# Kernel tuning notes

Measured on AMD Instinct MI355X. Metric: run time of the kernel, lower is better.

## Reference

```python
import jax, jax.numpy as jnp
import numpy as np

T = 100      # sequence length / output times
B = 2048     # batch
DT = 0.02    # euler step == spacing of ts -> one step per interval
CLAMP = 6.0
LOG2PI = float(np.log(2.0 * np.pi))
sp = jax.nn.softplus


def setup_inputs() -> dict:
    key = jax.random.key(0)
    ks = jax.random.split(key, 20)
    rn = lambda k, s, sc=1.0: jax.random.normal(k, s, dtype=jnp.float32) * sc
    inp = {}
    inp['xs'] = rn(ks[0], (T, B, 3, 50))
    inp['ts'] = jnp.arange(T, dtype=jnp.float32) * DT
    inp['eps0'] = rn(ks[1], (B, 6))
    inp['dW'] = rn(ks[2], (T - 1, B, 6)) * np.sqrt(DT)  # Brownian increments ~ N(0, dt)
    # encoder: 150->30->30->15
    inp['eW1'] = rn(ks[3], (150, 30), 150 ** -0.5); inp['eb1'] = jnp.zeros((30,), jnp.float32)
    inp['eW2'] = rn(ks[4], (30, 30), 30 ** -0.5);   inp['eb2'] = jnp.zeros((30,), jnp.float32)
    inp['eW3'] = rn(ks[5], (30, 15), 30 ** -0.5);   inp['eb3'] = jnp.zeros((15,), jnp.float32)
    # decoder: 6->30->30->100
    inp['dcW1'] = rn(ks[6], (6, 30), 6 ** -0.5);    inp['dcb1'] = jnp.zeros((30,), jnp.float32)
    inp['dcW2'] = rn(ks[7], (30, 30), 30 ** -0.5);  inp['dcb2'] = jnp.zeros((30,), jnp.float32)
    inp['dcW3'] = rn(ks[8], (30, 100), 30 ** -0.5); inp['dcb3'] = jnp.zeros((100,), jnp.float32)
    # f_net: (6+1+3)=10 -> 30 -> 6
    inp['fW1'] = rn(ks[9], (10, 30), 10 ** -0.5);   inp['fb1'] = jnp.zeros((30,), jnp.float32)
    inp['fW2'] = rn(ks[10], (30, 6), 30 ** -0.5);   inp['fb2'] = jnp.zeros((6,), jnp.float32)
    # h_net: (6+1)=7 -> 30 -> 6
    inp['hW1'] = rn(ks[11], (7, 30), 7 ** -0.5);    inp['hb1'] = jnp.zeros((30,), jnp.float32)
    inp['hW2'] = rn(ks[12], (30, 6), 30 ** -0.5);   inp['hb2'] = jnp.zeros((6,), jnp.float32)
    # 6 g_nets stacked: 2 -> 30 -> 1 (sigmoid)
    inp['gW1'] = rn(ks[13], (6, 2, 30), 2 ** -0.5); inp['gb1'] = jnp.zeros((6, 30), jnp.float32)
    inp['gW2'] = rn(ks[14], (6, 30, 1), 30 ** -0.5); inp['gb2'] = jnp.zeros((6, 1), jnp.float32)
    inp['pz0_mean'] = jnp.zeros((1, 6), jnp.float32)
    inp['pz0_logstd'] = jnp.zeros((1, 6), jnp.float32)
    return inp


def _forward(xs, ts, eps0, dW, eW1, eb1, eW2, eb2, eW3, eb3,
             dcW1, dcb1, dcW2, dcb2, dcW3, dcb3,
             fW1, fb1, fW2, fb2, hW1, hb1, hW2, hb2,
             gW1, gb1, gW2, gb2, pz0_mean, pz0_logstd):
    # ---- encoder on time-reversed xs ----
    xse = jnp.flip(xs, 0).reshape(T, B, 150)
    e = sp(xse @ eW1 + eb1)
    e = sp(e @ eW2 + eb2)
    e = e @ eW3 + eb3                         # [T,B,15]
    qz0_mean = e[-1, :, :6]
    qz0_logstd = e[-1, :, 6:12]
    ctx = jnp.flip(e[..., 12:15], 0)           # [T,B,3]

    z0 = qz0_mean + jnp.exp(jnp.clip(qz0_logstd, -CLAMP, CLAMP)) * eps0

    # ---- Euler-Maruyama with logqp (one step per ts interval) ----
    def step(z, sc):
        k, dWk = sc
        t = ts[k]
        dtk = ts[k + 1] - ts[k]
        c = ctx[jnp.minimum(k + 1, T - 1)]     # searchsorted(ts, t, right=True) clamped
        tb = jnp.broadcast_to(t, (B, 1)).astype(z.dtype)
        f = sp(jnp.concatenate([tb, z, c], 1) @ fW1 + fb1) @ fW2 + fb2
        h = sp(jnp.concatenate([tb, z], 1) @ hW1 + hb1) @ hW2 + hb2
        gin = jnp.stack([jnp.broadcast_to(t, (B, 6)).astype(z.dtype), z], -1)  # [B,6,2]
        gh = sp(jnp.einsum('bdi,dih->bdh', gin, gW1) + gb1)
        g = jax.nn.sigmoid(jnp.einsum('bdh,dho->bdo', gh, gW2) + gb2)[..., 0]  # [B,6]
        u = (f - h) / g
        logr = 0.5 * jnp.sum(u * u, axis=1) * dtk   # [B]
        zn = z + f * dtk + g * dWk
        return zn, (zn, logr)

    _, (zs_tail, log_ratio) = jax.lax.scan(step, z0, (jnp.arange(T - 1), dW))
    zs = jnp.concatenate([z0[None], zs_tail], 0)   # [T,B,6]

    # ---- decoder + likelihood ----
    d = sp(zs @ dcW1 + dcb1)
    d = sp(d @ dcW2 + dcb2)
    d = d @ dcW3 + dcb3                        # [T,B,100]
    xm, xl = d[..., :50], d[..., 50:]
    xsig = jnp.exp(jnp.clip(xl, -CLAMP, CLAMP))
    tgt = xs[:, :, -1, :]
    lp = -0.5 * ((tgt - xm) / xsig) ** 2 - jnp.log(xsig) - 0.5 * LOG2PI
    log_pxs = jnp.mean(jnp.sum(lp, axis=(0, 2)))

    # ---- KL(q(z0)||p(z0)) + path term ----
    sq = jnp.exp(jnp.clip(qz0_logstd, -CLAMP, CLAMP))
    spz = jnp.exp(jnp.clip(pz0_logstd, -CLAMP, CLAMP))
    kl = jnp.log(spz / sq) + (sq ** 2 + (qz0_mean - pz0_mean) ** 2) / (2.0 * spz ** 2) - 0.5
    logqp0 = jnp.mean(jnp.sum(kl, axis=1))
    logqp_path = jnp.mean(jnp.sum(log_ratio, axis=0))
    return log_pxs, logqp0 + logqp_path


def reference(xs, ts, eps0, dW, eW1, eb1, eW2, eb2, eW3, eb3,
              dcW1, dcb1, dcW2, dcb2, dcW3, dcb3,
              fW1, fb1, fW2, fb2, hW1, hb1, hW2, hb2,
              gW1, gb1, gW2, gb2, pz0_mean, pz0_logstd):
    return _forward(xs, ts, eps0, dW, eW1, eb1, eW2, eb2, eW3, eb3,
                    dcW1, dcb1, dcW2, dcb2, dcW3, dcb3,
                    fW1, fb1, fW2, fb2, hW1, hb1, hW2, hb2,
                    gW1, gb1, gW2, gb2, pz0_mean, pz0_logstd)
```

## Files before the change

### kernel.cpp

```cpp
#include <hip/hip_runtime.h>
#include <hip/hip_bf16.h>
#include <math.h>

#define Tn 100
#define Bn 2048

typedef int v2i __attribute__((ext_vector_type(2)));
typedef _Float16 h2v __attribute__((ext_vector_type(2)));

__device__ __forceinline__ float sp_f(float x) {
    float e = __expf(-fabsf(x));
    return fmaxf(x, 0.f) + __logf(1.f + e);
}
__device__ __forceinline__ float clamp6(float x) {
    return fminf(fmaxf(x, -6.f), 6.f);
}
__device__ __forceinline__ unsigned int packh2(float a, float b) {
    h2v h; h.x = (_Float16)a; h.y = (_Float16)b;
    return __builtin_bit_cast(unsigned int, h);
}
__device__ __forceinline__ float dot2f(unsigned int a, unsigned int b, float c) {
#if __has_builtin(__builtin_amdgcn_fdot2)
    return __builtin_amdgcn_fdot2(__builtin_bit_cast(h2v, a),
                                  __builtin_bit_cast(h2v, b), c, false);
#else
    h2v ha = __builtin_bit_cast(h2v, a), hb = __builtin_bit_cast(h2v, b);
    return fmaf((float)ha.y, (float)hb.y, fmaf((float)ha.x, (float)hb.x, c));
#endif
}

__device__ __forceinline__ float dpp_xor1(float x) {
    return __int_as_float(__builtin_amdgcn_mov_dpp(__float_as_int(x), 0xB1, 0xF, 0xF, 1));
}
__device__ __forceinline__ float dpp_xor2(float x) {
    return __int_as_float(__builtin_amdgcn_mov_dpp(__float_as_int(x), 0x4E, 0xF, 0xF, 1));
}
__device__ __forceinline__ float dpp_hmirror(float x) {
    return __int_as_float(__builtin_amdgcn_mov_dpp(__float_as_int(x), 0x141, 0xF, 0xF, 1));
}
__device__ __forceinline__ float dpp_ror8(float x) {
    return __int_as_float(__builtin_amdgcn_mov_dpp(__float_as_int(x), 0x128, 0xF, 0xF, 1));
}
template <int OFF>
__device__ __forceinline__ float swz(float x) {
    return __int_as_float(__builtin_amdgcn_ds_swizzle(__float_as_int(x), OFF));
}
__device__ __forceinline__ float xor16_sum(float x) {
#if __has_builtin(__builtin_amdgcn_permlane16_swap)
    v2i r = __builtin_amdgcn_permlane16_swap(__float_as_int(x), __float_as_int(x), false, false);
    return __int_as_float(r[0]) + __int_as_float(r[1]);
#else
    return x + swz<0x401F>(x);
#endif
}
__device__ __forceinline__ float other_half(float x) {
#if __has_builtin(__builtin_amdgcn_permlane32_swap)
    v2i r = __builtin_amdgcn_permlane32_swap(__float_as_int(x), __float_as_int(x), false, false);
    return (__int_as_float(r[0]) + __int_as_float(r[1])) - x;
#else
    return __shfl_xor(x, 32);
#endif
}

__device__ __forceinline__ void rowd2(float* ha, float* hb, const unsigned int* wrow,
                                      unsigned int xa, unsigned int xb) {
#pragma unroll
    for (int q = 0; q < 7; ++q) {
        uint4 wv = *(const uint4*)(wrow + 4 * q);
        ha[4 * q + 0] = dot2f(xa, wv.x, ha[4 * q + 0]);
        hb[4 * q + 0] = dot2f(xb, wv.x, hb[4 * q + 0]);
        ha[4 * q + 1] = dot2f(xa, wv.y, ha[4 * q + 1]);
        hb[4 * q + 1] = dot2f(xb, wv.y, hb[4 * q + 1]);
        ha[4 * q + 2] = dot2f(xa, wv.z, ha[4 * q + 2]);
        hb[4 * q + 2] = dot2f(xb, wv.z, hb[4 * q + 2]);
        ha[4 * q + 3] = dot2f(xa, wv.w, ha[4 * q + 3]);
        hb[4 * q + 3] = dot2f(xb, wv.w, hb[4 * q + 3]);
    }
    uint2 wt = *(const uint2*)(wrow + 28);
    ha[28] = dot2f(xa, wt.x, ha[28]);
    hb[28] = dot2f(xb, wt.x, hb[28]);
    ha[29] = dot2f(xa, wt.y, ha[29]);
    hb[29] = dot2f(xb, wt.y, hb[29]);
}
__device__ __forceinline__ void dot30_2(const float* ha, const float* hb,
                                        const float* wrow, float& ra, float& rb) {
    float a0 = 0.f, a1 = 0.f, b0 = 0.f, b1 = 0.f;
#pragma unroll
    for (int q = 0; q < 7; ++q) {
        float4 wv = *(const float4*)(wrow + 4 * q);
        a0 = fmaf(ha[4 * q + 0], wv.x, a0);
        b0 = fmaf(hb[4 * q + 0], wv.x, b0);
        a1 = fmaf(ha[4 * q + 1], wv.y, a1);
        b1 = fmaf(hb[4 * q + 1], wv.y, b1);
        a0 = fmaf(ha[4 * q + 2], wv.z, a0);
        b0 = fmaf(hb[4 * q + 2], wv.z, b0);
        a1 = fmaf(ha[4 * q + 3], wv.w, a1);
        b1 = fmaf(hb[4 * q + 3], wv.w, b1);
    }
    float2 wt = *(const float2*)(wrow + 28);
    a0 = fmaf(ha[28], wt.x, a0);
    b0 = fmaf(hb[28], wt.x, b0);
    a1 = fmaf(ha[29], wt.y, a1);
    b1 = fmaf(hb[29], wt.y, b1);
    ra = a0 + a1; rb = b0 + b1;
}
__device__ __forceinline__ void dot16p_2(const unsigned int* pa, const unsigned int* pb,
                                         const unsigned int* wrow, float& ra, float& rb) {
    float a0 = 0.f, a1 = 0.f, b0 = 0.f, b1 = 0.f;
#pragma unroll
    for (int q = 0; q < 4; ++q) {
        uint4 wv = *(const uint4*)(wrow + 4 * q);
        a0 = dot2f(pa[4 * q + 0], wv.x, a0);
        b0 = dot2f(pb[4 * q + 0], wv.x, b0);
        a1 = dot2f(pa[4 * q + 1], wv.y, a1);
        b1 = dot2f(pb[4 * q + 1], wv.y, b1);
        a0 = dot2f(pa[4 * q + 2], wv.z, a0);
        b0 = dot2f(pb[4 * q + 2], wv.z, b0);
        a1 = dot2f(pa[4 * q + 3], wv.w, a1);
        b1 = dot2f(pb[4 * q + 3], wv.w, b1);
    }
    ra = a0 + a1; rb = b0 + b1;
}

#define ENC_LOAD2(b0, b1, base)                                               \
    _Pragma("unroll")                                                         \
    for (int i = 0; i < 5; ++i) {                                             \
        b0[i] = *(const float2*)(x0 + (base) + 2 * i);                        \
        b1[i] = *(const float2*)(x1 + (base) + 2 * i);                        \
    }
#define ENC_COMP2(b0, b1, pb)                                                 \
    _Pragma("unroll")                                                         \
    for (int i = 0; i < 5; ++i) {                                             \
        unsigned int xa = packh2(b0[i].x, b0[i].y);                           \
        unsigned int xb = packh2(b1[i].x, b1[i].y);                           \
        rowd2(h1a, h1b, &wh1[((pb) + i) * 32], xa, xb);                       \
    }

__global__ __launch_bounds__(256) void enc_kernel(
    const float* __restrict__ xs,
    const float* __restrict__ eW1, const float* __restrict__ eb1,
    const float* __restrict__ eW2, const float* __restrict__ eb2,
    const float* __restrict__ eW3, const float* __restrict__ eb3,
    float* __restrict__ ctx, float* __restrict__ qm, float* __restrict__ qs)
{
    __shared__ __align__(16) unsigned int wh1[75 * 32];
    __shared__ __align__(16) unsigned int wh2[15 * 32];
    __shared__ __align__(16) float wf[555];

    for (int i = threadIdx.x; i < 75 * 30; i += 256) {
        int p = i / 30, j = i % 30;
        wh1[p * 32 + j] = packh2(eW1[(2 * p) * 30 + j], eW1[(2 * p + 1) * 30 + j]);
    }
    for (int i = threadIdx.x; i < 15 * 30; i += 256) {
        int p = i / 30, j = i % 30;
        wh2[p * 32 + j] = packh2(eW2[(2 * p) * 30 + j], eW2[(2 * p + 1) * 30 + j]);
    }
    if (threadIdx.x < 30) wf[threadIdx.x] = eb1[threadIdx.x];
    if (threadIdx.x >= 32 && threadIdx.x < 62) wf[30 + threadIdx.x - 32] = eb2[threadIdx.x - 32];
    for (int i = threadIdx.x; i < 90; i += 256) {
        int o = i / 30, j2 = i % 30;
        wf[60 + o * 32 + j2] = eW3[j2 * 15 + 12 + o];
    }
    for (int i = threadIdx.x; i < 360; i += 256) {
        int o = i / 30, j2 = i % 30;
        wf[156 + o * 32 + j2] = eW3[j2 * 15 + o];
    }
    if (threadIdx.x >= 64 && threadIdx.x < 79) wf[540 + threadIdx.x - 64] = eb3[threadIdx.x - 64];
    __syncthreads();

    int t = threadIdx.x;
    size_t base = (size_t)blockIdx.x * 512;
    size_t s0 = base + t, s1 = base + t + 256;
    const float* x0 = xs + s0 * 150;
    const float* x1 = xs + s1 * 150;

    float h1a[30], h1b[30];
#pragma unroll
    for (int j = 0; j < 30; ++j) { h1a[j] = wf[j]; h1b[j] = h1a[j]; }

    float2 A0[5], A1[5], B0[5], B1[5];
    ENC_LOAD2(A0, A1, 0)
    ENC_LOAD2(B0, B1, 10)
    int fb = 0;
#pragma unroll 1
    for (int it = 0; it < 6; ++it) {
        ENC_COMP2(A0, A1, fb / 2)
        ENC_LOAD2(A0, A1, fb + 20)
        ENC_COMP2(B0, B1, fb / 2 + 5)
        ENC_LOAD2(B0, B1, fb + 30)
        fb += 20;
    }
    ENC_COMP2(A0, A1, 60)
    ENC_LOAD2(A0, A1, 140)
    ENC_COMP2(B0, B1, 65)
    ENC_COMP2(A0, A1, 70)

#pragma unroll
    for (int j = 0; j < 30; ++j) { h1a[j] = sp_f(h1a[j]); h1b[j] = sp_f(h1b[j]); }

    unsigned int p1a[15], p1b[15];
#pragma unroll
    for (int p = 0; p < 15; ++p) {
        p1a[p] = packh2(h1a[2 * p], h1a[2 * p + 1]);
        p1b[p] = packh2(h1b[2 * p], h1b[2 * p + 1]);
    }
    float h2a[30], h2b[30];
#pragma unroll
    for (int j = 0; j < 30; ++j) { h2a[j] = wf[30 + j]; h2b[j] = h2a[j]; }
#pragma unroll
    for (int p = 0; p < 15; ++p)
        rowd2(h2a, h2b, &wh2[p * 32], p1a[p], p1b[p]);
#pragma unroll
    for (int j = 0; j < 30; ++j) { h2a[j] = sp_f(h2a[j]); h2b[j] = sp_f(h2b[j]); }

    float oa3[3], ob3[3];
#pragma unroll
    for (int o = 0; o < 3; ++o) {
        float ra, rb;
        dot30_2(h2a, h2b, &wf[60 + o * 32], ra, rb);
        oa3[o] = wf[540 + 12 + o] + ra;
        ob3[o] = wf[540 + 12 + o] + rb;
    }
    float* cp0 = ctx + s0 * 3;
    cp0[0] = oa3[0]; cp0[1] = oa3[1]; cp0[2] = oa3[2];
    float* cp1 = ctx + s1 * 3;
    cp1[0] = ob3[0]; cp1[1] = ob3[1]; cp1[2] = ob3[2];

    if (blockIdx.x < 4) {
#pragma unroll
        for (int o = 0; o < 12; ++o) {
            float ra, rb;
            dot30_2(h2a, h2b, &wf[156 + o * 32], ra, rb);
            float va = wf[540 + o] + ra, vb = wf[540 + o] + rb;
            if (o < 6) { qm[s0 * 6 + o] = va; qm[s1 * 6 + o] = vb; }
            else       { qs[s0 * 6 + o - 6] = va; qs[s1 * 6 + o - 6] = vb; }
        }
    }
}

__global__ __launch_bounds__(128, 4) void scan_kernel(
    const float* __restrict__ ts, const float* __restrict__ dWall,
    const float* __restrict__ fW1, const float* __restrict__ fb1,
    const float* __restrict__ fW2, const float* __restrict__ fb2,
    const float* __restrict__ hW1, const float* __restrict__ hb1,
    const float* __restrict__ hW2, const float* __restrict__ hb2,
    const float* __restrict__ gW1, const float* __restrict__ gb1,
    const float* __restrict__ gW2, const float* __restrict__ gb2,
    const float* __restrict__ ctx,
    const float* __restrict__ qm, const float* __restrict__ qs,
    const float* __restrict__ eps0, const float* __restrict__ pm,
    const float* __restrict__ ps,
    float* __restrict__ zsb, float* __restrict__ acc)
{
    int tid = threadIdx.x;
    int lane = tid & 63;
    int b = blockIdx.x;
    bool isA = tid < 64;

    __shared__ float sRec[99 * 12];
    __shared__ float exF[2][12];
    __shared__ float exG[2][8];

    for (int i = tid; i < 99 * 3; i += 128) {
        int k = i / 3, e = i % 3;
        float2 v = *(const float2*)(dWall + ((size_t)k * Bn + b) * 6 + e * 2);
        *(float2*)&sRec[k * 12 + e * 2] = v;
    }
    for (int i = tid; i < 99 * 3; i += 128) {
        int k = i / 3, e = i % 3;
        sRec[k * 12 + 6 + e] = ctx[((size_t)(k + 1) * Bn + b) * 3 + e];
    }
    for (int i = tid; i < 99; i += 128) {
        float t0 = ts[i], t1 = ts[i + 1];
        sRec[i * 12 + 9]  = 0.f;
        sRec[i * 12 + 10] = t0;
        sRec[i * 12 + 11] = t1 - t0;
    }

    float z[6];
    float zq = 0.f;
    float wl1[10], b1w, wl2[6], fb2v[6], hb2v[6];
    float gwa[4], gwb[4], gw2v[4], gbb[4], gb2v = 0.f, wselq = 0.f;
    int dL = 0;

    if (isA) {
        bool lower = lane < 32;
        int j = lane & 31;
        int jc = (j < 30) ? j : 29;
        bool jvalid = (j < 30);
#pragma unroll
        for (int i = 0; i < 10; ++i)
            wl1[i] = lower ? fW1[i * 30 + jc] : (i < 7 ? hW1[i * 30 + jc] : 0.f);
        b1w = lower ? fb1[jc] : hb1[jc];
#pragma unroll
        for (int d = 0; d < 6; ++d)
            wl2[d] = jvalid ? (lower ? fW2[jc * 6 + d] : hW2[jc * 6 + d]) : 0.f;
#pragma unroll
        for (int d = 0; d < 6; ++d) { fb2v[d] = fb2[d]; hb2v[d] = hb2[d]; }
#pragma unroll
        for (int d = 0; d < 6; ++d) {
            float m = qm[b * 6 + d];
            float sq = __expf(clamp6(qs[b * 6 + d]));
            z[d] = fmaf(sq, eps0[b * 6 + d], m);
        }
        if (tid == 0) {
            float* zp = zsb + (size_t)b * 6;
            *(float2*)(zp)     = make_float2(z[0], z[1]);
            *(float2*)(zp + 2) = make_float2(z[2], z[3]);
            *(float2*)(zp + 4) = make_float2(z[4], z[5]);
        }
    } else {
        int dL8 = lane >> 3;
        dL = (dL8 < 6) ? dL8 : 0;
        wselq = (dL8 < 6) ? 0.0625f : 0.f;
        int s = lane & 7;
#pragma unroll
        for (int u = 0; u < 4; ++u) {
            int jj = s + 8 * u;
            bool ok = (dL8 < 6) && (jj < 30);
            gwa[u]  = ok ? gW1[dL * 60 + jj] : 0.f;
            gwb[u]  = ok ? gW1[dL * 60 + 30 + jj] : 0.f;
            gw2v[u] = ok ? gW2[dL * 30 + jj] : 0.f;
            gbb[u]  = ok ? gb1[dL * 30 + jj] : 0.f;
        }
        gb2v = gb2[dL];
        {
            float m = qm[b * 6 + dL];
            float sq = __expf(clamp6(qs[b * 6 + dL]));
            zq = fmaf(sq, eps0[b * 6 + dL], m);
        }
        if (tid == 64) {
            float klsum = 0.f;
#pragma unroll
            for (int d = 0; d < 6; ++d) {
                float m = qm[b * 6 + d];
                float sq = __expf(clamp6(qs[b * 6 + d]));
                float spz = __expf(clamp6(ps[d]));
                float dm = m - pm[d];
                klsum += __logf(spz / sq) + (sq * sq + dm * dm) / (2.f * spz * spz) - 0.5f;
            }
            atomicAdd(&acc[1], klsum);
        }
    }

    __syncthreads();

    float pacc = 0.f;

    for (int k = 0; k < Tn - 1; ++k) {
        int kb = k & 1;

        if (isA) {
            float4 r0 = *(float4*)&sRec[k * 12];
            float4 r1 = *(float4*)&sRec[k * 12 + 4];
            float4 r2 = *(float4*)&sRec[k * 12 + 8];
            float t = r2.z, dt = r2.w;

            float a = fmaf(t, wl1[0], b1w);
#pragma unroll
            for (int i = 0; i < 6; ++i) a = fmaf(z[i], wl1[1 + i], a);
            a = fmaf(r1.z, wl1[7], a);
            a = fmaf(r1.w, wl1[8], a);
            a = fmaf(r2.x, wl1[9], a);
            float hid = sp_f(a);

            float pp[6];
#pragma unroll
            for (int d = 0; d < 6; ++d) pp[d] = hid * wl2[d];
#pragma unroll
            for (int d = 0; d < 6; ++d) pp[d] += dpp_xor1(pp[d]);
#pragma unroll
            for (int d = 0; d < 6; ++d) pp[d] += dpp_xor2(pp[d]);
#pragma unroll
            for (int d = 0; d < 6; ++d) pp[d] += dpp_hmirror(pp[d]);
#pragma unroll
            for (int d = 0; d < 6; ++d) pp[d] += dpp_ror8(pp[d]);
#pragma unroll
            for (int d = 0; d < 6; ++d) pp[d] = xor16_sum(pp[d]);
            float fvv[6], dfh[6];
            bool lower = lane < 32;
#pragma unroll
            for (int d = 0; d < 6; ++d) {
                float oth = other_half(pp[d]);
                float fsum = lower ? pp[d] : oth;
                float hsum = lower ? oth : pp[d];
                fvv[d] = fsum + fb2v[d];
                dfh[d] = fvv[d] - (hsum + hb2v[d]);
            }
            if (lane == 0) {
                *(float4*)&exF[kb][0] = make_float4(fvv[0], fvv[1], fvv[2], fvv[3]);
                *(float4*)&exF[kb][4] = make_float4(fvv[4], fvv[5], dfh[0], dfh[1]);
                *(float4*)&exF[kb][8] = make_float4(dfh[2], dfh[3], dfh[4], dfh[5]);
            }

            __syncthreads();

            float4 g03 = *(float4*)&exG[kb][0];
            float2 g45 = *(float2*)&exG[kb][4];
            float gl[6] = { g03.x, g03.y, g03.z, g03.w, g45.x, g45.y };
            float dwv[6] = { r0.x, r0.y, r0.z, r0.w, r1.x, r1.y };
#pragma unroll
            for (int d = 0; d < 6; ++d)
                z[d] = fmaf(gl[d], dwv[d], fmaf(fvv[d], dt, z[d]));

            if (tid == 0) {
                float* zp = zsb + ((size_t)(k + 1) * Bn + b) * 6;
                *(float2*)(zp)     = make_float2(z[0], z[1]);
                *(float2*)(zp + 2) = make_float2(z[2], z[3]);
                *(float2*)(zp + 4) = make_float2(z[4], z[5]);
            }
        } else {
            float2 tdt = *(float2*)&sRec[k * 12 + 10];
            float t = tdt.x, dt = tdt.y;
            float dwq = sRec[k * 12 + dL];

            float ga = 0.f;
#pragma unroll
            for (int u = 0; u < 4; ++u) {
                float pre = fmaf(t, gwa[u], gbb[u]);
                pre = fmaf(zq, gwb[u], pre);
                ga = fmaf(sp_f(pre), gw2v[u], ga);
            }
            ga += dpp_xor1(ga);
            ga += dpp_xor2(ga);
            ga += dpp_hmirror(ga);
            float gacc = ga + gb2v;
            float e = __expf(-gacc);
            float rg = 1.f + e;
            float gval = __builtin_amdgcn_rcpf(rg);
            if ((lane & 7) == 0 && (lane >> 3) < 6)
                exG[kb][dL] = gval;

            __syncthreads();

            float fq  = exF[kb][dL];
            float dfq = exF[kb][6 + dL];
            float u = dfq * rg;
            pacc = fmaf(wselq * dt, u * u, pacc);
            zq = fmaf(gval, dwq, fmaf(fq, dt, zq));
        }
    }
    if (!isA) {
#pragma unroll
        for (int mm = 1; mm <= 32; mm <<= 1) pacc += __shfl_xor(pacc, mm);
        if (tid == 64) atomicAdd(&acc[2], pacc);
    }
}

#define DEC_TLOAD(b0, b1, base)                                               \
    _Pragma("unroll")                                                         \
    for (int i = 0; i < 5; ++i) {                                             \
        b0[i] = *(const float2*)(tg0 + (base) + 2 * i);                       \
        b1[i] = *(const float2*)(tg1 + (base) + 2 * i);                       \
    }
#define DEC_LCOMP(b0, b1, base)                                               \
    _Pragma("unroll")                                                         \
    for (int i = 0; i < 10; ++i) {                                            \
        int ff = (base) + i;                                                  \
        float dma, dmb, dla, dlb;                                             \
        dot16p_2(p2a, p2b, &wh3[ff * 16], dma, dmb);                          \
        dot16p_2(p2a, p2b, &wh3[(50 + ff) * 16], dla, dlb);                   \
        float xma = wd[256 + ff] + dma, xmb = wd[256 + ff] + dmb;             \
        float cla = clamp6(wd[256 + 50 + ff] + dla);                          \
        float clb = clamp6(wd[256 + 50 + ff] + dlb);                          \
        float tva = (i & 1) ? b0[i >> 1].y : b0[i >> 1].x;                    \
        float tvb = (i & 1) ? b1[i >> 1].y : b1[i >> 1].x;                    \
        float ua = (tva - xma) * __expf(-cla);                                \
        float ub = (tvb - xmb) * __expf(-clb);                                \
        lpa += -0.5f * ua * ua - cla - 0.91893853320467274f;                  \
        lpb += -0.5f * ub * ub - clb - 0.91893853320467274f;                  \
    }

__global__ __launch_bounds__(256) void dec_kernel(
    const float* __restrict__ zsb, const float* __restrict__ xs,
    const float* __restrict__ dcW1, const float* __restrict__ dcb1,
    const float* __restrict__ dcW2, const float* __restrict__ dcb2,
    const float* __restrict__ dcW3, const float* __restrict__ dcb3,
    float* __restrict__ acc)
{
    __shared__ __align__(16) float wd[356];
    __shared__ __align__(16) unsigned int wh2d[15 * 32];
    __shared__ __align__(16) unsigned int wh3[100 * 16];

    for (int i = threadIdx.x; i < 180; i += 256) wd[(i / 30) * 32 + (i % 30)] = dcW1[i];
    if (threadIdx.x < 30) wd[192 + threadIdx.x] = dcb1[threadIdx.x];
    if (threadIdx.x >= 32 && threadIdx.x < 62) wd[224 + threadIdx.x - 32] = dcb2[threadIdx.x - 32];
    for (int i = threadIdx.x; i < 100; i += 256) wd[256 + i] = dcb3[i];
    for (int i = threadIdx.x; i < 15 * 30; i += 256) {
        int p = i / 30, j = i % 30;
        wh2d[p * 32 + j] = packh2(dcW2[(2 * p) * 30 + j], dcW2[(2 * p + 1) * 30 + j]);
    }
    for (int i = threadIdx.x; i < 100 * 16; i += 256) {
        int ff = i / 16, p = i % 16;
        wh3[i] = (p < 15) ? packh2(dcW3[(2 * p) * 100 + ff], dcW3[(2 * p + 1) * 100 + ff]) : 0u;
    }
    __syncthreads();

    int t = threadIdx.x;
    size_t base = (size_t)blockIdx.x * 512;
    size_t s0 = base + t, s1 = base + t + 256;

    float za[6], zb[6];
    {
        const float* zp0 = zsb + s0 * 6;
        const float* zp1 = zsb + s1 * 6;
#pragma unroll
        for (int i = 0; i < 3; ++i) {
            float2 v0 = *(const float2*)(zp0 + 2 * i);
            float2 v1 = *(const float2*)(zp1 + 2 * i);
            za[2 * i] = v0.x; za[2 * i + 1] = v0.y;
            zb[2 * i] = v1.x; zb[2 * i + 1] = v1.y;
        }
    }

    float h1a[30], h1b[30];
#pragma unroll
    for (int j = 0; j < 30; ++j) { h1a[j] = wd[192 + j]; h1b[j] = h1a[j]; }
#pragma unroll
    for (int i = 0; i < 6; ++i) {
        float via = za[i], vib = zb[i];
        const float* wrow = &wd[i * 32];
#pragma unroll
        for (int q = 0; q < 7; ++q) {
            float4 wv = *(const float4*)(wrow + 4 * q);
            h1a[4 * q + 0] = fmaf(via, wv.x, h1a[4 * q + 0]);
            h1b[4 * q + 0] = fmaf(vib, wv.x, h1b[4 * q + 0]);
            h1a[4 * q + 1] = fmaf(via, wv.y, h1a[4 * q + 1]);
            h1b[4 * q + 1] = fmaf(vib, wv.y, h1b[4 * q + 1]);
            h1a[4 * q + 2] = fmaf(via, wv.z, h1a[4 * q + 2]);
            h1b[4 * q + 2] = fmaf(vib, wv.z, h1b[4 * q + 2]);
            h1a[4 * q + 3] = fmaf(via, wv.w, h1a[4 * q + 3]);
            h1b[4 * q + 3] = fmaf(vib, wv.w, h1b[4 * q + 3]);
        }
        float2 wt = *(const float2*)(wrow + 28);
        h1a[28] = fmaf(via, wt.x, h1a[28]);
        h1b[28] = fmaf(vib, wt.x, h1b[28]);
        h1a[29] = fmaf(via, wt.y, h1a[29]);
        h1b[29] = fmaf(vib, wt.y, h1b[29]);
    }
#pragma unroll
    for (int j = 0; j < 30; ++j) { h1a[j] = sp_f(h1a[j]); h1b[j] = sp_f(h1b[j]); }

    unsigned int p1a[15], p1b[15];
#pragma unroll
    for (int p = 0; p < 15; ++p) {
        p1a[p] = packh2(h1a[2 * p], h1a[2 * p + 1]);
        p1b[p] = packh2(h1b[2 * p], h1b[2 * p + 1]);
    }
    float h2a[30], h2b[30];
#pragma unroll
    for (int j = 0; j < 30; ++j) { h2a[j] = wd[224 + j]; h2b[j] = h2a[j]; }
#pragma unroll
    for (int p = 0; p < 15; ++p)
        rowd2(h2a, h2b, &wh2d[p * 32], p1a[p], p1b[p]);
#pragma unroll
    for (int j = 0; j < 30; ++j) { h2a[j] = sp_f(h2a[j]); h2b[j] = sp_f(h2b[j]); }

    unsigned int p2a[16], p2b[16];
#pragma unroll
    for (int p = 0; p < 15; ++p) {
        p2a[p] = packh2(h2a[2 * p], h2a[2 * p + 1]);
        p2b[p] = packh2(h2b[2 * p], h2b[2 * p + 1]);
    }
    p2a[15] = 0u; p2b[15] = 0u;

    const float* tg0 = xs + s0 * 150 + 100;
    const float* tg1 = xs + s1 * 150 + 100;
    float lpa = 0.f, lpb = 0.f;
    float2 TA0[5], TA1[5], TB0[5], TB1[5];
    DEC_TLOAD(TA0, TA1, 0)
    DEC_TLOAD(TB0, TB1, 10)
    DEC_LCOMP(TA0, TA1, 0)
    DEC_TLOAD(TA0, TA1, 20)
    DEC_LCOMP(TB0, TB1, 10)
    DEC_TLOAD(TB0, TB1, 30)
    DEC_LCOMP(TA0, TA1, 20)
    DEC_TLOAD(TA0, TA1, 40)
    DEC_LCOMP(TB0, TB1, 30)
    DEC_LCOMP(TA0, TA1, 40)

    float lpacc = lpa + lpb;
#pragma unroll
    for (int mm = 1; mm <= 32; mm <<= 1) lpacc += __shfl_xor(lpacc, mm);
    __shared__ float red[4];
    if ((threadIdx.x & 63) == 0) red[threadIdx.x >> 6] = lpacc;
    __syncthreads();
    if (threadIdx.x == 0) atomicAdd(&acc[0], red[0] + red[1] + red[2] + red[3]);
}

__global__ void final_kernel(const float* __restrict__ acc, float* __restrict__ out)
{
    out[0] = acc[0] * (1.f / (float)Bn);
    out[1] = (acc[1] + acc[2]) * (1.f / (float)Bn);
}

extern "C" void kernel_launch(void* const* d_in, const int* in_sizes, int n_in,
                              void* d_out, int out_size, void* d_ws, size_t ws_size,
                              hipStream_t stream)
{
    const float* xs   = (const float*)d_in[0];
    const float* ts   = (const float*)d_in[1];
    const float* eps0 = (const float*)d_in[2];
    const float* dW   = (const float*)d_in[3];
    const float* eW1  = (const float*)d_in[4];
    const float* eb1  = (const float*)d_in[5];
    const float* eW2  = (const float*)d_in[6];
    const float* eb2  = (const float*)d_in[7];
    const float* eW3  = (const float*)d_in[8];
    const float* eb3  = (const float*)d_in[9];
    const float* dcW1 = (const float*)d_in[10];
    const float* dcb1 = (const float*)d_in[11];
    const float* dcW2 = (const float*)d_in[12];
    const float* dcb2 = (const float*)d_in[13];
    const float* dcW3 = (const float*)d_in[14];
    const float* dcb3 = (const float*)d_in[15];
    const float* fW1  = (const float*)d_in[16];
    const float* fb1  = (const float*)d_in[17];
    const float* fW2  = (const float*)d_in[18];
    const float* fb2  = (const float*)d_in[19];
    const float* hW1  = (const float*)d_in[20];
    const float* hb1  = (const float*)d_in[21];
    const float* hW2  = (const float*)d_in[22];
    const float* hb2  = (const float*)d_in[23];
    const float* gW1  = (const float*)d_in[24];
    const float* gb1  = (const float*)d_in[25];
    const float* gW2  = (const float*)d_in[26];
    const float* gb2  = (const float*)d_in[27];
    const float* pm   = (const float*)d_in[28];
    const float* ps   = (const float*)d_in[29];

    float* ws  = (float*)d_ws;
    float* acc = ws;
    float* ctx = ws + 16;
    float* qm  = ctx + 614400;
    float* qs  = qm + 12288;
    float* zs  = qs + 12288;
    float* out = (float*)d_out;

    hipMemsetAsync(acc, 0, 16 * sizeof(float), stream);
    enc_kernel<<<400, 256, 0, stream>>>(xs, eW1, eb1, eW2, eb2, eW3, eb3, ctx, qm, qs);
    scan_kernel<<<2048, 128, 0, stream>>>(ts, dW, fW1, fb1, fW2, fb2, hW1, hb1,
                                          hW2, hb2, gW1, gb1, gW2, gb2, ctx,
                                          qm, qs, eps0, pm, ps, zs, acc);
    dec_kernel<<<400, 256, 0, stream>>>(zs, xs, dcW1, dcb1, dcW2, dcb2, dcW3, dcb3, acc);
    final_kernel<<<1, 1, 0, stream>>>(acc, out);
}
```

Baseline: 244.0 us.

## Process two batch elements per scan block to add ILP and halve syncs

Each scan block now advances two independent SDE trajectories at once, interleaving their f/h and g network evaluations, and the grid shrinks from 2048 to 1024 blocks. This is meant to hide the latency of the serial per-step dependency chain (DPP reductions, transcendentals, barriers) with independent work, and to halve the total number of block-level barriers. The cost is higher register and LDS use per thread, which may lower occupancy, and fewer blocks to spread across the CUs. The first-layer dot product is also split into two partial accumulators to shorten the dependency chain.

After: 253.3 us. 3.8% more time.

```diff
diff --git a/kernel.cpp b/kernel.cpp
--- a/kernel.cpp
+++ b/kernel.cpp
@@ -254,31 +254,30 @@
 {
     int tid = threadIdx.x;
     int lane = tid & 63;
-    int b = blockIdx.x;
+    int b0c = blockIdx.x * 2;
     bool isA = tid < 64;
 
-    __shared__ float sRec[99 * 12];
-    __shared__ float exF[2][12];
-    __shared__ float exG[2][8];
-
-    for (int i = tid; i < 99 * 3; i += 128) {
-        int k = i / 3, e = i % 3;
-        float2 v = *(const float2*)(dWall + ((size_t)k * Bn + b) * 6 + e * 2);
-        *(float2*)&sRec[k * 12 + e * 2] = v;
-    }
-    for (int i = tid; i < 99 * 3; i += 128) {
-        int k = i / 3, e = i % 3;
-        sRec[k * 12 + 6 + e] = ctx[((size_t)(k + 1) * Bn + b) * 3 + e];
+    __shared__ float sRec[99 * 24];
+    __shared__ float exF[2][2][12];
+    __shared__ float exG[2][2][8];
+
+    for (int i = tid; i < 99 * 6; i += 128) {
+        int k = i / 6, r = i % 6, c = r / 3, e = r % 3;
+        float2 v = *(const float2*)(dWall + ((size_t)k * Bn + b0c + c) * 6 + e * 2);
+        *(float2*)&sRec[k * 24 + c * 12 + e * 2] = v;
+    }
+    for (int i = tid; i < 99 * 6; i += 128) {
+        int k = i / 6, r = i % 6, c = r / 3, e = r % 3;
+        sRec[k * 24 + c * 12 + 6 + e] = ctx[((size_t)(k + 1) * Bn + b0c + c) * 3 + e];
     }
     for (int i = tid; i < 99; i += 128) {
         float t0 = ts[i], t1 = ts[i + 1];
-        sRec[i * 12 + 9]  = 0.f;
-        sRec[i * 12 + 10] = t0;
-        sRec[i * 12 + 11] = t1 - t0;
-    }
-
-    float z[6];
-    float zq = 0.f;
+        sRec[i * 24 + 9]  = 0.f; sRec[i * 24 + 10] = t0; sRec[i * 24 + 11] = t1 - t0;
+        sRec[i * 24 + 21] = 0.f; sRec[i * 24 + 22] = t0; sRec[i * 24 + 23] = t1 - t0;
+    }
+
+    float z0[6], z1[6];
+    float zq0 = 0.f, zq1 = 0.f;
     float wl1[10], b1w, wl2[6], fb2v[6], hb2v[6];
     float gwa[4], gwb[4], gw2v[4], gbb[4], gb2v = 0.f, wselq = 0.f;
     int dL = 0;
@@ -299,15 +298,18 @@
         for (int d = 0; d < 6; ++d) { fb2v[d] = fb2[d]; hb2v[d] = hb2[d]; }
 #pragma unroll
         for (int d = 0; d < 6; ++d) {
-            float m = qm[b * 6 + d];
-            float sq = __expf(clamp6(qs[b * 6 + d]));
-            z[d] = fmaf(sq, eps0[b * 6 + d], m);
+            float m0 = qm[b0c * 6 + d];
+            float s0 = __expf(clamp6(qs[b0c * 6 + d]));
+            z0[d] = fmaf(s0, eps0[b0c * 6 + d], m0);
+            float m1 = qm[(b0c + 1) * 6 + d];
+            float s1 = __expf(clamp6(qs[(b0c + 1) * 6 + d]));
+            z1[d] = fmaf(s1, eps0[(b0c + 1) * 6 + d], m1);
         }
         if (tid == 0) {
-            float* zp = zsb + (size_t)b * 6;
-            *(float2*)(zp)     = make_float2(z[0], z[1]);
-            *(float2*)(zp + 2) = make_float2(z[2], z[3]);
-            *(float2*)(zp + 4) = make_float2(z[4], z[5]);
+            float* zp = zsb + (size_t)b0c * 6;
+            *(float4*)(zp)     = make_float4(z0[0], z0[1], z0[2], z0[3]);
+            *(float4*)(zp + 4) = make_float4(z0[4], z0[5], z1[0], z1[1]);
+            *(float4*)(zp + 8) = make_float4(z1[2], z1[3], z1[4], z1[5]);
         }
     } else {
         int dL8 = lane >> 3;
@@ -325,19 +327,25 @@
         }
         gb2v = gb2[dL];
         {
-            float m = qm[b * 6 + dL];
-            float sq = __expf(clamp6(qs[b * 6 + dL]));
-            zq = fmaf(sq, eps0[b * 6 + dL], m);
+            float m0 = qm[b0c * 6 + dL];
+            float s0 = __expf(clamp6(qs[b0c * 6 + dL]));
+            zq0 = fmaf(s0, eps0[b0c * 6 + dL], m0);
+            float m1 = qm[(b0c + 1) * 6 + dL];
+            float s1 = __expf(clamp6(qs[(b0c + 1) * 6 + dL]));
+            zq1 = fmaf(s1, eps0[(b0c + 1) * 6 + dL], m1);
         }
         if (tid == 64) {
             float klsum = 0.f;
 #pragma unroll
-            for (int d = 0; d < 6; ++d) {
-                float m = qm[b * 6 + d];
-                float sq = __expf(clamp6(qs[b * 6 + d]));
-                float spz = __expf(clamp6(ps[d]));
-                float dm = m - pm[d];
-                klsum += __logf(spz / sq) + (sq * sq + dm * dm) / (2.f * spz * spz) - 0.5f;
+            for (int c = 0; c < 2; ++c) {
+#pragma unroll
+                for (int d = 0; d < 6; ++d) {
+                    float m = qm[(b0c + c) * 6 + d];
+                    float sq = __expf(clamp6(qs[(b0c + c) * 6 + d]));
+                    float spz = __expf(clamp6(ps[d]));
+                    float dm = m - pm[d];
+                    klsum += __logf(spz / sq) + (sq * sq + dm * dm) / (2.f * spz * spz) - 0.5f;
+                }
             }
             atomicAdd(&acc[1], klsum);
         }
@@ -351,93 +359,130 @@
         int kb = k & 1;
 
         if (isA) {
-            float4 r0 = *(float4*)&sRec[k * 12];
-            float4 r1 = *(float4*)&sRec[k * 12 + 4];
-            float4 r2 = *(float4*)&sRec[k * 12 + 8];
-            float t = r2.z, dt = r2.w;
-
-            float a = fmaf(t, wl1[0], b1w);
-#pragma unroll
-            for (int i = 0; i < 6; ++i) a = fmaf(z[i], wl1[1 + i], a);
-            a = fmaf(r1.z, wl1[7], a);
-            a = fmaf(r1.w, wl1[8], a);
-            a = fmaf(r2.x, wl1[9], a);
-            float hid = sp_f(a);
-
-            float pp[6];
-#pragma unroll
-            for (int d = 0; d < 6; ++d) pp[d] = hid * wl2[d];
-#pragma unroll
-            for (int d = 0; d < 6; ++d) pp[d] += dpp_xor1(pp[d]);
-#pragma unroll
-            for (int d = 0; d < 6; ++d) pp[d] += dpp_xor2(pp[d]);
-#pragma unroll
-            for (int d = 0; d < 6; ++d) pp[d] += dpp_hmirror(pp[d]);
-#pragma unroll
-            for (int d = 0; d < 6; ++d) pp[d] += dpp_ror8(pp[d]);
-#pragma unroll
-            for (int d = 0; d < 6; ++d) pp[d] = xor16_sum(pp[d]);
-            float fvv[6], dfh[6];
+            float4 r0a = *(float4*)&sRec[k * 24];
+            float4 r1a = *(float4*)&sRec[k * 24 + 4];
+            float4 r2a = *(float4*)&sRec[k * 24 + 8];
+            float4 r0b = *(float4*)&sRec[k * 24 + 12];
+            float4 r1b = *(float4*)&sRec[k * 24 + 16];
+            float4 r2b = *(float4*)&sRec[k * 24 + 20];
+            float t = r2a.z, dt = r2a.w;
+
+            float a00 = fmaf(t, wl1[0], b1w);
+            a00 = fmaf(z0[0], wl1[1], a00);
+            a00 = fmaf(z0[1], wl1[2], a00);
+            a00 = fmaf(z0[2], wl1[3], a00);
+            a00 = fmaf(z0[3], wl1[4], a00);
+            float a01 = z0[4] * wl1[5];
+            a01 = fmaf(z0[5], wl1[6], a01);
+            a01 = fmaf(r1a.z, wl1[7], a01);
+            a01 = fmaf(r1a.w, wl1[8], a01);
+            a01 = fmaf(r2a.x, wl1[9], a01);
+            float a10 = fmaf(t, wl1[0], b1w);
+            a10 = fmaf(z1[0], wl1[1], a10);
+            a10 = fmaf(z1[1], wl1[2], a10);
+            a10 = fmaf(z1[2], wl1[3], a10);
+            a10 = fmaf(z1[3], wl1[4], a10);
+            float a11 = z1[4] * wl1[5];
+            a11 = fmaf(z1[5], wl1[6], a11);
+            a11 = fmaf(r1b.z, wl1[7], a11);
+            a11 = fmaf(r1b.w, wl1[8], a11);
+            a11 = fmaf(r2b.x, wl1[9], a11);
+            float hid0 = sp_f(a00 + a01);
+            float hid1 = sp_f(a10 + a11);
+
+            float pp0[6], pp1[6];
+#pragma unroll
+            for (int d = 0; d < 6; ++d) { pp0[d] = hid0 * wl2[d]; pp1[d] = hid1 * wl2[d]; }
+#pragma unroll
+            for (int d = 0; d < 6; ++d) { pp0[d] += dpp_xor1(pp0[d]); pp1[d] += dpp_xor1(pp1[d]); }
+#pragma unroll
+            for (int d = 0; d < 6; ++d) { pp0[d] += dpp_xor2(pp0[d]); pp1[d] += dpp_xor2(pp1[d]); }
+#pragma unroll
+            for (int d = 0; d < 6; ++d) { pp0[d] += dpp_hmirror(pp0[d]); pp1[d] += dpp_hmirror(pp1[d]); }
+#pragma unroll
+            for (int d = 0; d < 6; ++d) { pp0[d] += dpp_ror8(pp0[d]); pp1[d] += dpp_ror8(pp1[d]); }
+#pragma unroll
+            for (int d = 0; d < 6; ++d) { pp0[d] = xor16_sum(pp0[d]); pp1[d] = xor16_sum(pp1[d]); }
+            float fvv0[6], fvv1[6];
             bool lower = lane < 32;
 #pragma unroll
             for (int d = 0; d < 6; ++d) {
-                float oth = other_half(pp[d]);
-                float fsum = lower ? pp[d] : oth;
-                float hsum = lower ? oth : pp[d];
-                fvv[d] = fsum + fb2v[d];
-                dfh[d] = fvv[d] - (hsum + hb2v[d]);
+                float oth0 = other_half(pp0[d]);
+                float fs0 = lower ? pp0[d] : oth0;
+                float hs0 = lower ? oth0 : pp0[d];
+                fvv0[d] = fs0 + fb2v[d];
+                float df0 = fvv0[d] - (hs0 + hb2v[d]);
+                float oth1 = other_half(pp1[d]);
+                float fs1 = lower ? pp1[d] : oth1;
+                float hs1 = lower ? oth1 : pp1[d];
+                fvv1[d] = fs1 + fb2v[d];
+                float df1 = fvv1[d] - (hs1 + hb2v[d]);
+                if (lane == 0) {
+                    exF[kb][0][d] = fvv0[d]; exF[kb][0][6 + d] = df0;
+                    exF[kb][1][d] = fvv1[d]; exF[kb][1][6 + d] = df1;
+                }
             }
-            if (lane == 0) {
-                *(float4*)&exF[kb][0] = make_float4(fvv[0], fvv[1], fvv[2], fvv[3]);
-                *(float4*)&exF[kb][4] = make_float4(fvv[4], fvv[5], dfh[0], dfh[1]);
-                *(float4*)&exF[kb][8] = make_float4(dfh[2], dfh[3], dfh[4], dfh[5]);
+
+            __syncthreads();
+
+            float4 g03a = *(float4*)&exG[kb][0][0];
+            float2 g45a = *(float2*)&exG[kb][0][4];
+            float4 g03b = *(float4*)&exG[kb][1][0];
+            float2 g45b = *(float2*)&exG[kb][1][4];
+            float gl0[6] = { g03a.x, g03a.y, g03a.z, g03a.w, g45a.x, g45a.y };
+            float gl1[6] = { g03b.x, g03b.y, g03b.z, g03b.w, g45b.x, g45b.y };
+            float dwv0[6] = { r0a.x, r0a.y, r0a.z, r0a.w, r1a.x, r1a.y };
+            float dwv1[6] = { r0b.x, r0b.y, r0b.z, r0b.w, r1b.x, r1b.y };
+#pragma unroll
+            for (int d = 0; d < 6; ++d) {
+                z0[d] = fmaf(gl0[d], dwv0[d], fmaf(fvv0[d], dt, z0[d]));
+                z1[d] = fmaf(gl1[d], dwv1[d], fmaf(fvv1[d], dt, z1[d]));
             }
 
-            __syncthreads();
-
-            float4 g03 = *(float4*)&exG[kb][0];
-            float2 g45 = *(float2*)&exG[kb][4];
-            float gl[6] = { g03.x, g03.y, g03.z, g03.w, g45.x, g45.y };
-            float dwv[6] = { r0.x, r0.y, r0.z, r0.w, r1.x, r1.y };
-#pragma unroll
-            for (int d = 0; d < 6; ++d)
-                z[d] = fmaf(gl[d], dwv[d], fmaf(fvv[d], dt, z[d]));
-
             if (tid == 0) {
-                float* zp = zsb + ((size_t)(k + 1) * Bn + b) * 6;
-                *(float2*)(zp)     = make_float2(z[0], z[1]);
-                *(float2*)(zp + 2) = make_float2(z[2], z[3]);
-                *(float2*)(zp + 4) = make_float2(z[4], z[5]);
+                float* zp = zsb + ((size_t)(k + 1) * Bn + b0c) * 6;
+                *(float4*)(zp)     = make_float4(z0[0], z0[1], z0[2], z0[3]);
+                *(float4*)(zp + 4) = make_float4(z0[4], z0[5], z1[0], z1[1]);
+                *(float4*)(zp + 8) = make_float4(z1[2], z1[3], z1[4], z1[5]);
             }
         } else {
-            float2 tdt = *(float2*)&sRec[k * 12 + 10];
+            float2 tdt = *(float2*)&sRec[k * 24 + 10];
             float t = tdt.x, dt = tdt.y;
-            float dwq = sRec[k * 12 + dL];
-
-            float ga = 0.f;
+            float dwq0 = sRec[k * 24 + dL];
+            float dwq1 = sRec[k * 24 + 12 + dL];
+
+            float ga0 = 0.f, ga1 = 0.f;
 #pragma unroll
             for (int u = 0; u < 4; ++u) {
-                float pre = fmaf(t, gwa[u], gbb[u]);
-                pre = fmaf(zq, gwb[u], pre);
-                ga = fmaf(sp_f(pre), gw2v[u], ga);
+                float prec = fmaf(t, gwa[u], gbb[u]);
+                float pre0 = fmaf(zq0, gwb[u], prec);
+                float pre1 = fmaf(zq1, gwb[u], prec);
+                ga0 = fmaf(sp_f(pre0), gw2v[u], ga0);
+                ga1 = fmaf(sp_f(pre1), gw2v[u], ga1);
             }
-            ga += dpp_xor1(ga);
-            ga += dpp_xor2(ga);
-            ga += dpp_hmirror(ga);
-            float gacc = ga + gb2v;
-            float e = __expf(-gacc);
-            float rg = 1.f + e;
-            float gval = __builtin_amdgcn_rcpf(rg);
-            if ((lane & 7) == 0 && (lane >> 3) < 6)
-                exG[kb][dL] = gval;
+            ga0 += dpp_xor1(ga0);   ga1 += dpp_xor1(ga1);
+            ga0 += dpp_xor2(ga0);   ga1 += dpp_xor2(ga1);
+            ga0 += dpp_hmirror(ga0); ga1 += dpp_hmirror(ga1);
+            float gacc0 = ga0 + gb2v, gacc1 = ga1 + gb2v;
+            float e0 = __expf(-gacc0), e1 = __expf(-gacc1);
+            float rg0 = 1.f + e0, rg1 = 1.f + e1;
+            float gval0 = __builtin_amdgcn_rcpf(rg0);
+            float gval1 = __builtin_amdgcn_rcpf(rg1);
+            if ((lane & 7) == 0 && (lane >> 3) < 6) {
+                exG[kb][0][dL] = gval0;
+                exG[kb][1][dL] = gval1;
+            }
 
             __syncthreads();
 
-            float fq  = exF[kb][dL];
-            float dfq = exF[kb][6 + dL];
-            float u = dfq * rg;
-            pacc = fmaf(wselq * dt, u * u, pacc);
-            zq = fmaf(gval, dwq, fmaf(fq, dt, zq));
+            float fq0  = exF[kb][0][dL];
+            float dfq0 = exF[kb][0][6 + dL];
+            float fq1  = exF[kb][1][dL];
+            float dfq1 = exF[kb][1][6 + dL];
+            float u0 = dfq0 * rg0, u1 = dfq1 * rg1;
+            pacc = fmaf(wselq * dt, fmaf(u0, u0, u1 * u1), pacc);
+            zq0 = fmaf(gval0, dwq0, fmaf(fq0, dt, zq0));
+            zq1 = fmaf(gval1, dwq1, fmaf(fq1, dt, zq1));
         }
     }
     if (!isA) {
@@ -639,7 +684,7 @@
 
     hipMemsetAsync(acc, 0, 16 * sizeof(float), stream);
     enc_kernel<<<400, 256, 0, stream>>>(xs, eW1, eb1, eW2, eb2, eW3, eb3, ctx, qm, qs);
-    scan_kernel<<<2048, 128, 0, stream>>>(ts, dW, fW1, fb1, fW2, fb2, hW1, hb1,
+    scan_kernel<<<1024, 128, 0, stream>>>(ts, dW, fW1, fb1, fW2, fb2, hW1, hb1,
                                           hW2, hb2, gW1, gb1, gW2, gb2, ctx,
                                           qm, qs, eps0, pm, ps, zs, acc);
     dec_kernel<<<400, 256, 0, stream>>>(zs, xs, dcW1, dcb1, dcW2, dcb2, dcW3, dcb3, acc);
```
